# Kernel tuning notes

Measured on AMD Instinct MI355X. Metric: run time of the kernel, lower is better.

The kernel has to match this reference:

```python
import jax, jax.numpy as jnp
import numpy as np

A0 = 0.5291772105638411
KE = 14.399645351950548
KEHALF = KE / 2.0


def _softplus_inverse(x):
    return float(np.log(np.expm1(x)))


def setup_inputs() -> dict:
    key = jax.random.key(0)
    k_nb, k_mask, k_z, k_r = jax.random.split(key, 4)
    B, A, K = 16, 1024, 1023
    neighbors = jax.random.randint(k_nb, (B, A, K), 0, A)
    neighbor_mask = (jax.random.uniform(k_mask, (B, A, K)) > 0.1).astype(jnp.float32)
    atomic_numbers = jax.random.randint(k_z, (B, A), 1, 95)
    r_ij = jax.random.uniform(k_r, (B, A, K), minval=0.5, maxval=10.0, dtype=jnp.float32)
    p = jnp.float32
    params = {
        "_adiv": jnp.full((1,), _softplus_inverse(1.0 / (0.8854 * A0)), p),
        "_apow": jnp.full((1,), _softplus_inverse(0.23), p),
        "_c1": jnp.full((1,), _softplus_inverse(0.1818), p),
        "_c2": jnp.full((1,), _softplus_inverse(0.5099), p),
        "_c3": jnp.full((1,), _softplus_inverse(0.2802), p),
        "_c4": jnp.full((1,), _softplus_inverse(0.02817), p),
        "_a1": jnp.full((1,), _softplus_inverse(3.2), p),
        "_a2": jnp.full((1,), _softplus_inverse(0.9423), p),
        "_a3": jnp.full((1,), _softplus_inverse(0.4028), p),
        "_a4": jnp.full((1,), _softplus_inverse(0.2016), p),
    }
    return dict(neighbors=neighbors, neighbor_mask=neighbor_mask,
                atomic_numbers=atomic_numbers, r_ij=r_ij, **params)


def reference(neighbors, neighbor_mask, atomic_numbers, r_ij,
              _adiv, _apow, _c1, _c2, _c3, _c4, _a1, _a2, _a3, _a4):
    sp = jax.nn.softplus
    B = neighbors.shape[0]
    Zf = atomic_numbers.astype(jnp.float32)            # [B, A]
    Zp = Zf ** sp(_apow)                               # [B, A] (param [1] broadcasts)
    bidx = jnp.arange(B)[:, None, None]                # batch index for gather
    # gather of symmetric pair quantities without materializing [B, A, A]:
    # a[b,i,j] = Zp[b,i] + Zp[b,j];  zizj[b,i,j] = Zf[b,i] * Zf[b,j]
    Zp_j = Zp[bidx, neighbors]                         # [B, A, K]
    Zf_j = Zf[bidx, neighbors]                         # [B, A, K]
    a = (Zp[:, :, None] + Zp_j) * sp(_adiv) * neighbor_mask
    zizj = Zf[:, :, None] * Zf_j * neighbor_mask
    # normalized mixture coefficients
    c1, c2, c3, c4 = sp(_c1), sp(_c2), sp(_c3), sp(_c4)
    csum = c1 + c2 + c3 + c4
    c1, c2, c3, c4 = c1 / csum, c2 / csum, c3 / csum, c4 / csum
    ar = a * r_ij
    f = (c1 * jnp.exp(-sp(_a1) * ar) + c2 * jnp.exp(-sp(_a2) * ar)
         + c3 * jnp.exp(-sp(_a3) * ar) + c4 * jnp.exp(-sp(_a4) * ar))
    valid = neighbor_mask != 0
    r_safe = jnp.where(valid, r_ij, 1.0)
    corr_ij = jnp.where(valid, KEHALF * f * zizj / r_safe, 0.0)
    return jnp.sum(corr_ij, axis=-1, keepdims=True)    # [B, A, 1]
```

## Files before the change

kernel.cpp:

```cpp
#include <hip/hip_runtime.h>
#include <math.h>

#define KEHALF_F 7.199822675975274f
#define A_ATOMS 1024
#define ROWS_PER_BLOCK 8

__device__ __forceinline__ float softplus_f(float x) {
    return log1pf(__expf(x));
}

__global__ __launch_bounds__(256) void zbl_fused_kernel(
    const int* __restrict__ neighbors,
    const float* __restrict__ neighbor_mask,
    const int* __restrict__ atomic_numbers,
    const float* __restrict__ r_ij,
    const float* __restrict__ p_adiv, const float* __restrict__ p_apow,
    const float* __restrict__ p_c1, const float* __restrict__ p_c2,
    const float* __restrict__ p_c3, const float* __restrict__ p_c4,
    const float* __restrict__ p_a1, const float* __restrict__ p_a2,
    const float* __restrict__ p_a3, const float* __restrict__ p_a4,
    float* __restrict__ out, int K)
{
    __shared__ float2 zz[A_ATOMS];

    const float sp_apow = softplus_f(p_apow[0]);
    const float sp_adiv = softplus_f(p_adiv[0]);
    float c1 = softplus_f(p_c1[0]), c2 = softplus_f(p_c2[0]);
    float c3 = softplus_f(p_c3[0]), c4 = softplus_f(p_c4[0]);
    const float inv_cs = 1.0f / (c1 + c2 + c3 + c4);
    c1 *= inv_cs; c2 *= inv_cs; c3 *= inv_cs; c4 *= inv_cs;
    const float a1 = softplus_f(p_a1[0]), a2 = softplus_f(p_a2[0]);
    const float a3 = softplus_f(p_a3[0]), a4 = softplus_f(p_a4[0]);

    const int row_base = blockIdx.x * ROWS_PER_BLOCK;
    const int b = row_base >> 10;
    const int* z_row = atomic_numbers + (b << 10);

    for (int t = threadIdx.x; t < A_ATOMS; t += 256) {
        float zf = (float)z_row[t];
        float zp = __expf(sp_apow * __logf(zf));
        zz[t] = make_float2(zf, zp);
    }
    __syncthreads();

    const int wid  = threadIdx.x >> 6;
    const int lane = threadIdx.x & 63;

    const int row0 = row_base + wid;
    const int row1 = row_base + wid + 4;
    const float2 zi0 = zz[row0 & (A_ATOMS - 1)];
    const float2 zi1 = zz[row1 & (A_ATOMS - 1)];

    const size_t base0 = (size_t)row0 * K;
    const size_t base1 = (size_t)row1 * K;
    const int*   nb0 = neighbors     + base0;
    const float* mk0 = neighbor_mask + base0;
    const float* rr0 = r_ij          + base0;
    const int*   nb1 = neighbors     + base1;
    const float* mk1 = neighbor_mask + base1;
    const float* rr1 = r_ij          + base1;

    float acc0 = 0.0f, acc1 = 0.0f;
    const int niter = (K + 63) >> 6;
    #pragma unroll 4
    for (int it = 0; it < niter; ++it) {
        const int k = (it << 6) + lane;
        if (k < K) {
            int   j0 = nb0[k];
            float m0 = mk0[k];
            float r0 = rr0[k];
            float2 zj0 = zz[j0];
            float ar0 = (zi0.y + zj0.y) * sp_adiv * m0 * r0;
            float f0  = c1 * __expf(-a1 * ar0) + c2 * __expf(-a2 * ar0)
                      + c3 * __expf(-a3 * ar0) + c4 * __expf(-a4 * ar0);
            acc0 += f0 * __fdividef(zi0.x * zj0.x * m0, r0);
            int   j1 = nb1[k];
            float m1 = mk1[k];
            float r1 = rr1[k];
            float2 zj1 = zz[j1];
            float ar1 = (zi1.y + zj1.y) * sp_adiv * m1 * r1;
            float f1  = c1 * __expf(-a1 * ar1) + c2 * __expf(-a2 * ar1)
                      + c3 * __expf(-a3 * ar1) + c4 * __expf(-a4 * ar1);
            acc1 += f1 * __fdividef(zi1.x * zj1.x * m1, r1);
        }
    }

    #pragma unroll
    for (int off = 32; off > 0; off >>= 1) {
        acc0 += __shfl_down(acc0, off, 64);
        acc1 += __shfl_down(acc1, off, 64);
    }
    if (lane == 0) {
        out[row0] = KEHALF_F * acc0;
        out[row1] = KEHALF_F * acc1;
    }
}

extern "C" void kernel_launch(void* const* d_in, const int* in_sizes, int n_in,
                              void* d_out, int out_size, void* d_ws, size_t ws_size,
                              hipStream_t stream) {
    const int*   neighbors      = (const int*)  d_in[0];
    const float* neighbor_mask  = (const float*)d_in[1];
    const int*   atomic_numbers = (const int*)  d_in[2];
    const float* r_ij           = (const float*)d_in[3];

    float* out = (float*)d_out;

    const int n = in_sizes[2];
    const int K = in_sizes[0] / n;

    zbl_fused_kernel<<<n / ROWS_PER_BLOCK, 256, 0, stream>>>(
        neighbors, neighbor_mask, atomic_numbers, r_ij,
        (const float*)d_in[4], (const float*)d_in[5],
        (const float*)d_in[6], (const float*)d_in[7],
        (const float*)d_in[8], (const float*)d_in[9],
        (const float*)d_in[10], (const float*)d_in[11],
        (const float*)d_in[12], (const float*)d_in[13],
        out, K);
}
```

Measured before the change: 235.3 us.

## Vectorize row loads with aligned int4/float4 and one row per wavefront

Each wavefront now handles a single row and reads neighbors, mask and r_ij as 16-byte vectors after a scalar alignment prologue, with head and tail elements handled by individual lanes. The block now covers 4 rows instead of 8, doubling the grid. It also folds sp_adiv into the cached Zp table, rewrites the exponentials as exp2f with log2e pre-scaled coefficients, and moves the KE/2 factor into the per-row Zi. The goal is fewer, wider memory transactions on a bandwidth-bound stream, at the cost of more prologue logic and less per-wave load overlap than the two-row interleave.

```diff
diff --git a/kernel.cpp b/kernel.cpp
--- a/kernel.cpp
+++ b/kernel.cpp
@@ -3,7 +3,7 @@
 
 #define KEHALF_F 7.199822675975274f
 #define A_ATOMS 1024
-#define ROWS_PER_BLOCK 8
+#define LOG2E_F 1.4426950408889634f
 
 __device__ __forceinline__ float softplus_f(float x) {
     return log1pf(__expf(x));
@@ -29,71 +29,80 @@
     float c3 = softplus_f(p_c3[0]), c4 = softplus_f(p_c4[0]);
     const float inv_cs = 1.0f / (c1 + c2 + c3 + c4);
     c1 *= inv_cs; c2 *= inv_cs; c3 *= inv_cs; c4 *= inv_cs;
-    const float a1 = softplus_f(p_a1[0]), a2 = softplus_f(p_a2[0]);
-    const float a3 = softplus_f(p_a3[0]), a4 = softplus_f(p_a4[0]);
+    const float b1 = -softplus_f(p_a1[0]) * LOG2E_F;
+    const float b2 = -softplus_f(p_a2[0]) * LOG2E_F;
+    const float b3 = -softplus_f(p_a3[0]) * LOG2E_F;
+    const float b4 = -softplus_f(p_a4[0]) * LOG2E_F;
 
-    const int row_base = blockIdx.x * ROWS_PER_BLOCK;
+    const int row_base = blockIdx.x << 2;
     const int b = row_base >> 10;
-    const int* z_row = atomic_numbers + (b << 10);
+    const int* zrow = atomic_numbers + (b << 10);
 
     for (int t = threadIdx.x; t < A_ATOMS; t += 256) {
-        float zf = (float)z_row[t];
-        float zp = __expf(sp_apow * __logf(zf));
+        float zf = (float)zrow[t];
+        float zp = exp2f(sp_apow * log2f(zf)) * sp_adiv;
         zz[t] = make_float2(zf, zp);
     }
     __syncthreads();
 
     const int wid  = threadIdx.x >> 6;
     const int lane = threadIdx.x & 63;
+    const int row  = row_base + wid;
 
-    const int row0 = row_base + wid;
-    const int row1 = row_base + wid + 4;
-    const float2 zi0 = zz[row0 & (A_ATOMS - 1)];
-    const float2 zi1 = zz[row1 & (A_ATOMS - 1)];
+    const float2 zi = zz[row & (A_ATOMS - 1)];
+    const float zix = KEHALF_F * zi.x;
+    const float ziy = zi.y;
 
-    const size_t base0 = (size_t)row0 * K;
-    const size_t base1 = (size_t)row1 * K;
-    const int*   nb0 = neighbors     + base0;
-    const float* mk0 = neighbor_mask + base0;
-    const float* rr0 = r_ij          + base0;
-    const int*   nb1 = neighbors     + base1;
-    const float* mk1 = neighbor_mask + base1;
-    const float* rr1 = r_ij          + base1;
+    const size_t base = (size_t)row * K;
+    const int f = (int)((4 - (int)(base & 3)) & 3);
+    const int ngroups = (K - f) >> 2;
+    const int tailc   = (K - f) & 3;
 
-    float acc0 = 0.0f, acc1 = 0.0f;
-    const int niter = (K + 63) >> 6;
-    #pragma unroll 4
-    for (int it = 0; it < niter; ++it) {
-        const int k = (it << 6) + lane;
-        if (k < K) {
-            int   j0 = nb0[k];
-            float m0 = mk0[k];
-            float r0 = rr0[k];
-            float2 zj0 = zz[j0];
-            float ar0 = (zi0.y + zj0.y) * sp_adiv * m0 * r0;
-            float f0  = c1 * __expf(-a1 * ar0) + c2 * __expf(-a2 * ar0)
-                      + c3 * __expf(-a3 * ar0) + c4 * __expf(-a4 * ar0);
-            acc0 += f0 * __fdividef(zi0.x * zj0.x * m0, r0);
-            int   j1 = nb1[k];
-            float m1 = mk1[k];
-            float r1 = rr1[k];
-            float2 zj1 = zz[j1];
-            float ar1 = (zi1.y + zj1.y) * sp_adiv * m1 * r1;
-            float f1  = c1 * __expf(-a1 * ar1) + c2 * __expf(-a2 * ar1)
-                      + c3 * __expf(-a3 * ar1) + c4 * __expf(-a4 * ar1);
-            acc1 += f1 * __fdividef(zi1.x * zj1.x * m1, r1);
-        }
+    const int*   nb = neighbors     + base;
+    const float* mk = neighbor_mask + base;
+    const float* rr = r_ij          + base;
+    const int4*   nb4 = (const int4*)  (nb + f);
+    const float4* mk4 = (const float4*)(mk + f);
+    const float4* rr4 = (const float4*)(rr + f);
+
+    float acc = 0.0f;
+
+#define ZBL_TERM(J, M, R)                                                   \
+    {                                                                       \
+        float2 zj = zz[(J)];                                                \
+        float ar = (ziy + zj.y) * (M) * (R);                                \
+        float fe = c1 * exp2f(b1 * ar) + c2 * exp2f(b2 * ar)                \
+                 + c3 * exp2f(b3 * ar) + c4 * exp2f(b4 * ar);               \
+        acc += fe * __fdividef(zix * zj.x * (M), (R));                      \
     }
 
+    #pragma unroll 2
+    for (int g = lane; g < ngroups; g += 64) {
+        int4   j4 = nb4[g];
+        float4 m4 = mk4[g];
+        float4 r4 = rr4[g];
+        ZBL_TERM(j4.x, m4.x, r4.x);
+        ZBL_TERM(j4.y, m4.y, r4.y);
+        ZBL_TERM(j4.z, m4.z, r4.z);
+        ZBL_TERM(j4.w, m4.w, r4.w);
+    }
+
+    int e = -1;
+    if (lane < f)                 e = lane;
+    else if (lane - f < tailc)    e = f + (ngroups << 2) + (lane - f);
+    if (e >= 0) {
+        int   j = nb[e];
+        float m = mk[e];
+        float r = rr[e];
+        ZBL_TERM(j, m, r);
+    }
+#undef ZBL_TERM
+
     #pragma unroll
-    for (int off = 32; off > 0; off >>= 1) {
-        acc0 += __shfl_down(acc0, off, 64);
-        acc1 += __shfl_down(acc1, off, 64);
-    }
-    if (lane == 0) {
-        out[row0] = KEHALF_F * acc0;
-        out[row1] = KEHALF_F * acc1;
-    }
+    for (int off = 32; off > 0; off >>= 1)
+        acc += __shfl_down(acc, off, 64);
+    if (lane == 0)
+        out[row] = acc;
 }
 
 extern "C" void kernel_launch(void* const* d_in, const int* in_sizes, int n_in,
@@ -109,7 +118,7 @@
     const int n = in_sizes[2];
     const int K = in_sizes[0] / n;
 
-    zbl_fused_kernel<<<n / ROWS_PER_BLOCK, 256, 0, stream>>>(
+    zbl_fused_kernel<<<n / 4, 256, 0, stream>>>(
         neighbors, neighbor_mask, atomic_numbers, r_ij,
         (const float*)d_in[4], (const float*)d_in[5],
         (const float*)d_in[6], (const float*)d_in[7],
```

Measured after the change: 222.1 us. 5.6% less time.
